# Performance work log

Hardware: AMD Instinct MI355X
Metric: run time of the kernel (lower is better)

Reference implementation:

```python
import jax, jax.numpy as jnp
import numpy as np

IN_FEATURES_LS = (8, 16, 32, 64, 128)
OUT_FEATURES = 512
MAX_FEAT = max(IN_FEATURES_LS)


def setup_inputs() -> dict:
    key = jax.random.key(0)
    k_x, k_idx, k_w, k_b = jax.random.split(key, 4)
    B, S = 16, 2048
    x = jax.random.normal(k_x, (B, S, MAX_FEAT), dtype=jnp.float32)
    # actual patch size per token: sample an index into in_features_ls
    idx = jax.random.randint(k_idx, (B, S), 0, len(IN_FEATURES_LS))
    in_feat_size = jnp.array(IN_FEATURES_LS, dtype=jnp.int64)[idx]
    weight = jax.random.normal(k_w, (len(IN_FEATURES_LS), OUT_FEATURES, MAX_FEAT), dtype=jnp.float32) * 0.05
    bias = jax.random.normal(k_b, (len(IN_FEATURES_LS), OUT_FEATURES), dtype=jnp.float32) * 0.05
    return {"x": x, "in_feat_size": in_feat_size, "weight": weight, "bias": bias}


def reference(x, in_feat_size, weight, bias):
    sizes = jnp.asarray(IN_FEATURES_LS)                       # [K]
    # mask padding columns of each expert's weight: [K, max_feat]
    feat_mask = (jnp.arange(MAX_FEAT)[None, :] < sizes[:, None]).astype(x.dtype)
    w = weight * feat_mask[:, None, :]                        # [K, out, max_feat]
    # all K projections computed unconditionally (faithful to original)
    y = jnp.einsum('bsi,koi->bsko', x, w) + bias              # [B, S, K, out]
    sel = (in_feat_size[..., None] == sizes).astype(x.dtype)  # [B, S, K] one-hot
    return jnp.einsum('bsko,bsk->bso', y, sel)                # [B, S, out]
```

## Files before the change

### kernel.cpp

```cpp
#include <hip/hip_runtime.h>

#define NEXP 5
#define MAXF 128
#define NOUT 512
#define NBMAX 256
#define PERMOFF (64 + NBMAX * NEXP)

typedef __attribute__((ext_vector_type(8))) short short8;
typedef __attribute__((ext_vector_type(4))) float floatx4;

__device__ __forceinline__ ushort f2bf(float f) {
    uint u = __float_as_uint(f);
    u += 0x7FFF + ((u >> 16) & 1);
    return (ushort)(u >> 16);
}


__global__ __launch_bounds__(256) void misl_hist(
    const int* __restrict__ feat, int* __restrict__ ws, int n) {
    __shared__ int lcnt[NEXP];
    const int tid = threadIdx.x;
    if (tid < NEXP) lcnt[tid] = 0;
    __syncthreads();
    const int t = blockIdx.x * 256 + tid;
    if (t < n) { const int e = __ffs(feat[t]) - 4; atomicAdd(&lcnt[e], 1); }
    __syncthreads();
    if (tid < NEXP) ws[64 + blockIdx.x * NEXP + tid] = lcnt[tid];
}

__global__ __launch_bounds__(256) void misl_rest(
    const int* __restrict__ feat, const float* __restrict__ x,
    const float* __restrict__ w, int* __restrict__ ws,
    ushort* __restrict__ wb, ushort* __restrict__ xb, int n, int nb) {
    const int tid = threadIdx.x;
    if ((int)blockIdx.x < nb) {
        __shared__ int ph[NBMAX * NEXP];
        __shared__ int lcnt[NEXP], lbase[NEXP], ltot[NEXP];
        for (int i = tid; i < nb * NEXP; i += 256) ph[i] = ws[64 + i];
        if (tid < NEXP) lcnt[tid] = 0;
        __syncthreads();
        if (tid < NEXP) {
            int tot = 0, pre = 0;
            for (int bb = 0; bb < nb; ++bb) {
                if (bb == (int)blockIdx.x) pre = tot;
                tot += ph[bb * NEXP + tid];
            }
            ltot[tid] = tot; lbase[tid] = pre;
        }
        __syncthreads();
        if (tid < NEXP) {
            int seg = 0;
            for (int e = 0; e < tid; ++e) seg += ltot[e];
            lbase[tid] += seg;
            if (blockIdx.x == 0) { ws[tid] = ltot[tid]; ws[8 + tid] = seg; }
        }
        __syncthreads();
        const int t = blockIdx.x * 256 + tid;
        if (t < n) {
            const int e = __ffs(feat[t]) - 4;
            const int r = atomicAdd(&lcnt[e], 1);
            ws[PERMOFF + lbase[e] + r] = t;
        }
    } else if ((int)blockIdx.x < nb + 160) {
        const int idx = ((int)blockIdx.x - nb) * 256 + tid;
        const int lane = idx & 63, nb16 = (idx >> 6) & 31;
        const int s = (idx >> 11) & 3, e = idx >> 13;
        if (e < NEXP) {
            const int ncol = nb16 * 16 + (lane & 15);
            const int k0 = s * 32 + (lane >> 4) * 8;
            const int K = 8 << e;
            const float* wr = w + ((size_t)e * NOUT + ncol) * MAXF + k0;
            short8 v;
            #pragma unroll
            for (int j = 0; j < 8; ++j)
                v[j] = (short)((k0 + j < K) ? f2bf(wr[j]) : (ushort)0);
            *(short8*)(wb + (size_t)idx * 8) = v;
        }
    } else {
        const int idx = ((int)blockIdx.x - nb - 160) * 256 + tid;
        if (idx < n * 16) {
            const float4 a = *(const float4*)(x + (size_t)idx * 8);
            const float4 c = *(const float4*)(x + (size_t)idx * 8 + 4);
            short8 v;
            v[0] = (short)f2bf(a.x); v[1] = (short)f2bf(a.y);
            v[2] = (short)f2bf(a.z); v[3] = (short)f2bf(a.w);
            v[4] = (short)f2bf(c.x); v[5] = (short)f2bf(c.y);
            v[6] = (short)f2bf(c.z); v[7] = (short)f2bf(c.w);
            *(short8*)(xb + (size_t)idx * 8) = v;
        }
    }
}

template <int NS>
__device__ __forceinline__ void mfma_run(
    const ushort* __restrict__ xb, const ushort* __restrict__ wbe,
    const float* __restrict__ be, const int* __restrict__ tokp, int rem,
    int lane, int n_base, float* __restrict__ out) {
    const int m = lane & 15, q = lane >> 4;
    const int nb16 = n_base >> 4;
    short8 bf[NS][4];
    #pragma unroll
    for (int s = 0; s < NS; ++s)
        #pragma unroll
        for (int bi = 0; bi < 4; ++bi)
            bf[s][bi] = *(const short8*)(wbe + ((size_t)((s * 32 + nb16 + bi)) * 64 + lane) * 8);
    float bv[4];
    #pragma unroll
    for (int bi = 0; bi < 4; ++bi) bv[bi] = be[n_base + bi * 16 + m];

    const int trips = (rem + 15) >> 4;
    for (int g = 0; g < trips; ++g) {
        const int base = g * 16;
        const int lim = rem - base;
        const int idx = (m < lim) ? m : lim - 1;
        const int tokv = tokp[base + idx];
        const ushort* xr = xb + (size_t)tokv * MAXF + q * 8;
        floatx4 acc[4];
        #pragma unroll
        for (int bi = 0; bi < 4; ++bi)
            acc[bi] = floatx4{bv[bi], bv[bi], bv[bi], bv[bi]};
        #pragma unroll
        for (int s = 0; s < NS; ++s) {
            const short8 af = *(const short8*)(xr + s * 32);
            #pragma unroll
            for (int bi = 0; bi < 4; ++bi)
                acc[bi] = __builtin_amdgcn_mfma_f32_16x16x32_bf16(af, bf[s][bi], acc[bi], 0, 0, 0);
        }
        #pragma unroll
        for (int r = 0; r < 4; ++r) {
            const int mi = q * 4 + r;
            const int tr = __shfl(tokv, mi, 16);
            if (mi < lim) {
                float* orow = out + (size_t)tr * NOUT + n_base + m;
                #pragma unroll
                for (int bi = 0; bi < 4; ++bi) orow[bi * 16] = acc[bi][r];
            }
        }
    }
}

__global__ __launch_bounds__(256) void misl_main(
    const ushort* __restrict__ xb, const ushort* __restrict__ wb,
    const float* __restrict__ b, const int* __restrict__ ws,
    float* __restrict__ out) {
    const int g = blockIdx.x >> 1;
    const int half = blockIdx.x & 1;
    const int c[NEXP] = {ws[0], ws[1], ws[2], ws[3], ws[4]};
    const int sg[NEXP] = {ws[8], ws[9], ws[10], ws[11], ws[12]};

    int gb = 0, e = -1, lgs = 0;
    #pragma unroll
    for (int j = 0; j < NEXP; ++j) {
        const int ee = 4 - j;
        const int ng = (c[ee] + 63) >> 6;
        if (e < 0 && g < gb + ng) { e = ee; lgs = g - gb; }
        gb += ng;
    }
    if (e < 0) return;

    int rem = c[e] - lgs * 64;
    if (rem > 64) rem = 64;
    const int* tokp = ws + PERMOFF + sg[e] + lgs * 64;
    const int lane = threadIdx.x & 63;
    const int wave = threadIdx.x >> 6;
    const int n_base = half * 256 + wave * 64;
    const ushort* wbe = wb + (size_t)e * 4 * 32 * 64 * 8;
    const float* be = b + e * NOUT;

    switch (e) {
        case 0: mfma_run<1>(xb, wbe, be, tokp, rem, lane, n_base, out); break;
        case 1: mfma_run<1>(xb, wbe, be, tokp, rem, lane, n_base, out); break;
        case 2: mfma_run<1>(xb, wbe, be, tokp, rem, lane, n_base, out); break;
        case 3: mfma_run<2>(xb, wbe, be, tokp, rem, lane, n_base, out); break;
        case 4: mfma_run<4>(xb, wbe, be, tokp, rem, lane, n_base, out); break;
    }
}

extern "C" void kernel_launch(void* const* d_in, const int* in_sizes, int n_in,
                              void* d_out, int out_size, void* d_ws, size_t ws_size,
                              hipStream_t stream) {
    const float* x    = (const float*)d_in[0];
    const int*   feat = (const int*)d_in[1];
    const float* w    = (const float*)d_in[2];
    const float* b    = (const float*)d_in[3];
    float* out = (float*)d_out;
    int*   ws  = (int*)d_ws;

    const int n  = in_sizes[1];
    const int nb = (n + 255) / 256;

    const size_t wb_off = (((size_t)(PERMOFF + n)) * 4 + 255) & ~(size_t)255;
    ushort* wb = (ushort*)((char*)d_ws + wb_off);
    const size_t xb_off = (wb_off + (size_t)NEXP * 4 * 32 * 64 * 8 * 2 + 255) & ~(size_t)255;
    ushort* xb = (ushort*)((char*)d_ws + xb_off);

    misl_hist<<<nb, 256, 0, stream>>>(feat, ws, n);
    const int cvb = (n * 16 + 255) / 256;
    misl_rest<<<nb + 160 + cvb, 256, 0, stream>>>(feat, x, w, ws, wb, xb, n, nb);
    misl_main<<<((n + 63) / 64 + NEXP) * 2, 256, 0, stream>>>(xb, wb, b, ws, out);
}
```

Before: 100.0 us.

## Replace histogram pre-pass and scan with global atomic bucket offsets

Removes the separate histogram kernel and the per-block serial prefix scan over block histograms. Each block now reserves its slot in a per-expert bucket with a global atomicAdd on the expert counters, which a memset zeroes first. The permutation buffer is laid out as NEXP regions of size n. The main GEMM kernel also moves from two 256-thread blocks per token group to one 512-thread block covering all 512 outputs. Token order within each expert becomes nondeterministic and the permutation buffer grows, while one kernel launch and a serial dependency are removed.

```diff
diff --git a/kernel.cpp b/kernel.cpp
--- a/kernel.cpp
+++ b/kernel.cpp
@@ -3,8 +3,7 @@
 #define NEXP 5
 #define MAXF 128
 #define NOUT 512
-#define NBMAX 256
-#define PERMOFF (64 + NBMAX * NEXP)
+#define PERMOFF 64
 
 typedef __attribute__((ext_vector_type(8))) short short8;
 typedef __attribute__((ext_vector_type(4))) float floatx4;
@@ -16,51 +15,25 @@
 }
 
 
-__global__ __launch_bounds__(256) void misl_hist(
-    const int* __restrict__ feat, int* __restrict__ ws, int n) {
-    __shared__ int lcnt[NEXP];
-    const int tid = threadIdx.x;
-    if (tid < NEXP) lcnt[tid] = 0;
-    __syncthreads();
-    const int t = blockIdx.x * 256 + tid;
-    if (t < n) { const int e = __ffs(feat[t]) - 4; atomicAdd(&lcnt[e], 1); }
-    __syncthreads();
-    if (tid < NEXP) ws[64 + blockIdx.x * NEXP + tid] = lcnt[tid];
-}
-
-__global__ __launch_bounds__(256) void misl_rest(
+__global__ __launch_bounds__(256) void misl_prep(
     const int* __restrict__ feat, const float* __restrict__ x,
     const float* __restrict__ w, int* __restrict__ ws,
     ushort* __restrict__ wb, ushort* __restrict__ xb, int n, int nb) {
     const int tid = threadIdx.x;
     if ((int)blockIdx.x < nb) {
-        __shared__ int ph[NBMAX * NEXP];
-        __shared__ int lcnt[NEXP], lbase[NEXP], ltot[NEXP];
-        for (int i = tid; i < nb * NEXP; i += 256) ph[i] = ws[64 + i];
+        __shared__ int lcnt[NEXP], lbase[NEXP];
         if (tid < NEXP) lcnt[tid] = 0;
         __syncthreads();
-        if (tid < NEXP) {
-            int tot = 0, pre = 0;
-            for (int bb = 0; bb < nb; ++bb) {
-                if (bb == (int)blockIdx.x) pre = tot;
-                tot += ph[bb * NEXP + tid];
-            }
-            ltot[tid] = tot; lbase[tid] = pre;
+        const int t = blockIdx.x * 256 + tid;
+        int e = 0, r = 0;
+        if (t < n) {
+            e = __ffs(feat[t]) - 4;
+            r = atomicAdd(&lcnt[e], 1);
         }
         __syncthreads();
-        if (tid < NEXP) {
-            int seg = 0;
-            for (int e = 0; e < tid; ++e) seg += ltot[e];
-            lbase[tid] += seg;
-            if (blockIdx.x == 0) { ws[tid] = ltot[tid]; ws[8 + tid] = seg; }
-        }
+        if (tid < NEXP) lbase[tid] = atomicAdd(&ws[8 + tid], lcnt[tid]);
         __syncthreads();
-        const int t = blockIdx.x * 256 + tid;
-        if (t < n) {
-            const int e = __ffs(feat[t]) - 4;
-            const int r = atomicAdd(&lcnt[e], 1);
-            ws[PERMOFF + lbase[e] + r] = t;
-        }
+        if (t < n) ws[PERMOFF + e * n + lbase[e] + r] = t;
     } else if ((int)blockIdx.x < nb + 160) {
         const int idx = ((int)blockIdx.x - nb) * 256 + tid;
         const int lane = idx & 63, nb16 = (idx >> 6) & 31;
@@ -103,7 +76,7 @@
     for (int s = 0; s < NS; ++s)
         #pragma unroll
         for (int bi = 0; bi < 4; ++bi)
-            bf[s][bi] = *(const short8*)(wbe + ((size_t)((s * 32 + nb16 + bi)) * 64 + lane) * 8);
+            bf[s][bi] = *(const short8*)(wbe + ((size_t)(s * 32 + nb16 + bi) * 64 + lane) * 8);
     float bv[4];
     #pragma unroll
     for (int bi = 0; bi < 4; ++bi) bv[bi] = be[n_base + bi * 16 + m];
@@ -139,14 +112,12 @@
     }
 }
 
-__global__ __launch_bounds__(256) void misl_main(
+__global__ __launch_bounds__(512) void misl_main(
     const ushort* __restrict__ xb, const ushort* __restrict__ wb,
     const float* __restrict__ b, const int* __restrict__ ws,
-    float* __restrict__ out) {
-    const int g = blockIdx.x >> 1;
-    const int half = blockIdx.x & 1;
-    const int c[NEXP] = {ws[0], ws[1], ws[2], ws[3], ws[4]};
-    const int sg[NEXP] = {ws[8], ws[9], ws[10], ws[11], ws[12]};
+    float* __restrict__ out, int n) {
+    const int g = blockIdx.x;
+    const int c[NEXP] = {ws[8], ws[9], ws[10], ws[11], ws[12]};
 
     int gb = 0, e = -1, lgs = 0;
     #pragma unroll
@@ -160,10 +131,10 @@
 
     int rem = c[e] - lgs * 64;
     if (rem > 64) rem = 64;
-    const int* tokp = ws + PERMOFF + sg[e] + lgs * 64;
+    const int* tokp = ws + PERMOFF + e * n + lgs * 64;
     const int lane = threadIdx.x & 63;
     const int wave = threadIdx.x >> 6;
-    const int n_base = half * 256 + wave * 64;
+    const int n_base = wave * 64;
     const ushort* wbe = wb + (size_t)e * 4 * 32 * 64 * 8;
     const float* be = b + e * NOUT;
 
@@ -189,13 +160,13 @@
     const int n  = in_sizes[1];
     const int nb = (n + 255) / 256;
 
-    const size_t wb_off = (((size_t)(PERMOFF + n)) * 4 + 255) & ~(size_t)255;
+    const size_t wb_off = (((size_t)(PERMOFF + (size_t)NEXP * n) * 4) + 255) & ~(size_t)255;
     ushort* wb = (ushort*)((char*)d_ws + wb_off);
     const size_t xb_off = (wb_off + (size_t)NEXP * 4 * 32 * 64 * 8 * 2 + 255) & ~(size_t)255;
     ushort* xb = (ushort*)((char*)d_ws + xb_off);
 
-    misl_hist<<<nb, 256, 0, stream>>>(feat, ws, n);
+    hipMemsetAsync(ws, 0, 64 * sizeof(int), stream);
     const int cvb = (n * 16 + 255) / 256;
-    misl_rest<<<nb + 160 + cvb, 256, 0, stream>>>(feat, x, w, ws, wb, xb, n, nb);
-    misl_main<<<((n + 63) / 64 + NEXP) * 2, 256, 0, stream>>>(xb, wb, b, ws, out);
+    misl_prep<<<nb + 160 + cvb, 256, 0, stream>>>(feat, x, w, ws, wb, xb, n, nb);
+    misl_main<<<(n + 63) / 64 + NEXP, 512, 0, stream>>>(xb, wb, b, ws, out, n);
 }
```

Result: faster. 96.77 us (-3.2%).
